# Kernel tuning notes

Measured on AMD Instinct MI355X. Metric: run time of the kernel, lower is better.

The kernel has to match this reference:

```python
import jax, jax.numpy as jnp
import numpy as np

B, N, D_IN, H, D_H, D_OUT = 2, 1024, 1024, 16, 64, 1024
NEG = -1e9


def skew_relative(QE_t):
    # QE_t: [B, H, N, 2N-1] -> [B, H, N, N] via the pad/reshape skew trick
    b, h, n = QE_t.shape[0], QE_t.shape[1], QE_t.shape[2]
    x = jnp.pad(QE_t, ((0, 0), (0, 0), (0, 0), (0, 1)))          # [B,H,N,2N]
    x = x.reshape(b, h, -1)                                       # [B,H,2N^2]
    x = jnp.pad(x, ((0, 0), (0, 0), (0, n - 1)))                  # [B,H,(N+1)(2N-1)]
    x = x.reshape(b, h, n + 1, 2 * n - 1)
    return x[:, :, :n, -n:]


def setup_inputs() -> dict:
    key = jax.random.key(0)
    ks = jax.random.split(key, 8)
    x = jax.random.normal(ks[0], (B, N, D_IN), dtype=jnp.float32)
    E_rel = jax.random.normal(ks[1], (2 * N - 1, D_H), dtype=jnp.float32)
    # additive causal mask [1,1,N,N]
    causal = jnp.tril(jnp.ones((N, N), dtype=bool))
    mask = jnp.where(causal, 0.0, NEG).astype(jnp.float32)[None, None]
    s = 1.0 / np.sqrt(D_IN)
    Wq = jax.random.normal(ks[2], (D_IN, H * D_H), dtype=jnp.float32) * s
    Wk = jax.random.normal(ks[3], (D_IN, H * D_H), dtype=jnp.float32) * s
    Wv = jax.random.normal(ks[4], (D_IN, H * D_H), dtype=jnp.float32) * s
    Wo = jax.random.normal(ks[5], (H * D_H, D_OUT), dtype=jnp.float32) * (1.0 / np.sqrt(H * D_H))
    bo = jnp.zeros((D_OUT,), dtype=jnp.float32)
    return {"x": x, "E_rel": E_rel, "mask": mask, "Wq": Wq, "Wk": Wk, "Wv": Wv, "Wo": Wo, "bo": bo}


def reference(x, E_rel, mask, Wq, Wk, Wv, Wo, bo):
    b = x.shape[0]
    scale = 1.0 / np.sqrt(D_H)
    # project and split heads -> [B, H, N, d]
    Q = (x @ Wq).reshape(b, -1, H, D_H).transpose(0, 2, 1, 3)
    K = (x @ Wk).reshape(b, -1, H, D_H).transpose(0, 2, 1, 3)
    V = (x @ Wv).reshape(b, -1, H, D_H).transpose(0, 2, 1, 3)
    attn = jnp.einsum('bhnd,bhmd->bhnm', Q, K)                    # [B,H,N,N]
    QE_t = jnp.einsum('bhnd,rd->bhnr', Q, E_rel)                  # [B,H,N,2N-1]
    attn = (attn + skew_relative(QE_t)) * scale + mask
    attn = jax.nn.softmax(attn, axis=-1)
    out = jnp.einsum('bhnm,bhmd->bhnd', attn, V)                  # [B,H,N,d]
    out = out.transpose(0, 2, 1, 3).reshape(b, -1, H * D_H)
    return out @ Wo + bo  # dropout is identity at inference
```

## Files before the change

kernel.cpp:

```cpp
#include <hip/hip_runtime.h>
#include <cstdint>
#include <cstddef>

typedef __bf16 bf16;
typedef __bf16 bf16x8 __attribute__((ext_vector_type(8)));
typedef float  f32x4  __attribute__((ext_vector_type(4)));

#define MFMA16(a,b,c) __builtin_amdgcn_mfma_f32_16x16x32_bf16((a),(b),(c),0,0,0)

__device__ __forceinline__ void gload_lds16(const bf16* g, bf16* l) {
  __builtin_amdgcn_global_load_lds((__attribute__((address_space(1))) void*)(g),
                                   (__attribute__((address_space(3))) void*)(l),
                                   16, 0, 0);
}

__global__ void cast_bf16_k(const float* __restrict__ src, bf16* __restrict__ dst, int n) {
  int i = (blockIdx.x * blockDim.x + threadIdx.x) * 4;
  if (i >= n) return;
  float4 v = *(const float4*)(src + i);
  dst[i + 0] = (bf16)v.x;
  dst[i + 1] = (bf16)v.y;
  dst[i + 2] = (bf16)v.z;
  dst[i + 3] = (bf16)v.w;
}

__global__ void transpose4_k(const float* __restrict__ W0, const float* __restrict__ W1,
                             const float* __restrict__ W2, const float* __restrict__ W3,
                             bf16* __restrict__ dst_base) {
  const int z = blockIdx.z;
  const float* src = (z == 0) ? W0 : (z == 1) ? W1 : (z == 2) ? W2 : W3;
  bf16* dst = dst_base + (size_t)z * (1024 * 1024);
  __shared__ float t[32][33];
  const int c0 = blockIdx.x * 32, r0 = blockIdx.y * 32;
  const int x = threadIdx.x, y = threadIdx.y;
  #pragma unroll
  for (int j = 0; j < 32; j += 8) t[y + j][x] = src[(size_t)(r0 + y + j) * 1024 + c0 + x];
  __syncthreads();
  #pragma unroll
  for (int j = 0; j < 32; j += 8)
    dst[(size_t)(c0 + y + j) * 1024 + r0 + x] = (bf16)t[x][y + j];
}

template <int NI>
__global__ __launch_bounds__(256) void gemm_k(
    const bf16* __restrict__ A, const bf16* __restrict__ Bt,
    bf16* __restrict__ QKV, float* __restrict__ Of,
    const float* __restrict__ bias, const int mode) {
  constexpr int K = 1024;
  const int row0 = blockIdx.x * 64;
  const int col0 = blockIdx.y * (NI * 64);

  __shared__ bf16 As[2][64 * 64];
  __shared__ bf16 Bs[2][NI * 64 * 64];

  const int tid = threadIdx.x;
  const int lane = tid & 63;
  const int wid = tid >> 6;
  const int lr = lane & 15;
  const int g  = lane >> 4;
  const int srow = lane >> 3;
  const int scol = ((lane & 7) ^ srow) * 8;

  f32x4 acc[4][NI];
  #pragma unroll
  for (int a = 0; a < 4; ++a)
    #pragma unroll
    for (int b = 0; b < NI; ++b) acc[a][b] = (f32x4){0.f, 0.f, 0.f, 0.f};

  auto stg = [&](int bb, int k0_) {
    #pragma unroll
    for (int q = 0; q < 2; ++q)
      gload_lds16(A + (size_t)(row0 + wid * 16 + q * 8 + srow) * K + k0_ + scol,
                  &As[bb][(wid * 16 + q * 8) * 64]);
    #pragma unroll
    for (int q = 0; q < 2 * NI; ++q)
      gload_lds16(Bt + (size_t)(col0 + wid * NI * 16 + q * 8 + srow) * K + k0_ + scol,
                  &Bs[bb][(wid * NI * 16 + q * 8) * 64]);
  };

  stg(0, 0);
  for (int t = 0; t < K / 64; ++t) {
    __syncthreads();
    if (t + 1 < K / 64) stg((t + 1) & 1, (t + 1) * 64);
    const bf16* as = &As[t & 1][0];
    const bf16* bs = &Bs[t & 1][0];
    bf16x8 af[4][2], bfv[NI][2];
    #pragma unroll
    for (int mi = 0; mi < 4; ++mi)
      #pragma unroll
      for (int kk = 0; kk < 2; ++kk)
        af[mi][kk] = *(const bf16x8*)&as[(mi * 16 + lr) * 64 + ((kk * 32 + g * 8) ^ ((lr & 7) << 3))];
    #pragma unroll
    for (int ni = 0; ni < NI; ++ni)
      #pragma unroll
      for (int kk = 0; kk < 2; ++kk)
        bfv[ni][kk] = *(const bf16x8*)&bs[(wid * NI * 16 + ni * 16 + lr) * 64 +
                                          ((kk * 32 + g * 8) ^ ((lr & 7) << 3))];
    #pragma unroll
    for (int mi = 0; mi < 4; ++mi)
      #pragma unroll
      for (int ni = 0; ni < NI; ++ni)
        #pragma unroll
        for (int kk = 0; kk < 2; ++kk)
          acc[mi][ni] = MFMA16(af[mi][kk], bfv[ni][kk], acc[mi][ni]);
  }

  #pragma unroll
  for (int mi = 0; mi < 4; ++mi) {
    #pragma unroll
    for (int ni = 0; ni < NI; ++ni) {
      #pragma unroll
      for (int r = 0; r < 4; ++r) {
        const int row = row0 + mi * 16 + g * 4 + r;
        const int col = col0 + wid * NI * 16 + ni * 16 + lr;
        const float v = acc[mi][ni][r];
        if (mode == 2) {
          Of[(size_t)row * 1024 + col] = v + bias[col];
        } else {
          const int b = row >> 10, i = row & 1023;
          const int which = col >> 10, cc = col & 1023;
          const int h = cc >> 6, d = cc & 63;
          if (which < 2)
            QKV[(size_t)which * 2097152 + (((size_t)(b * 16 + h)) * 1024 + i) * 64 + d] = (bf16)v;
          else
            QKV[(size_t)2 * 2097152 + (((size_t)(b * 16 + h)) * 64 + d) * 1024 + i] = (bf16)v;
        }
      }
    }
  }
}

__device__ const int CH_QB[36] = {7,7,7,7,7,7,7, 6,6,6,6,6,6, 5,5,5,5,5, 4,4,4,4,
                                  3,3,3, 2,2, 1, 0,1,2,3,4,5,6,7};
__device__ const int CH_K0[36] = {0,2,4,6,8,10,12, 0,2,4,6,8,10, 0,2,4,6,8, 0,2,4,6,
                                  0,2,4, 0,2, 0, 0,2,4,6,8,10,12,14};
__device__ const int QB_P0[8] = {0,1,3,6,10,15,21,28};

__global__ __launch_bounds__(512, 6) void attn_kernel(
    const bf16* __restrict__ Qh, const bf16* __restrict__ Kh,
    const bf16* __restrict__ Vt, const bf16* __restrict__ Eb,
    float* __restrict__ OP, float* __restrict__ LP) {
  constexpr int N = 1024;
  const int flat = blockIdx.y * 36 + blockIdx.x;
  const int task = (flat & 7) * 144 + (flat >> 3);
  const int bh = task / 36;
  const int ch = task - bh * 36;
  const int qb = CH_QB[ch];
  const int kb0 = CH_K0[ch];
  const int i0 = qb * 128;

  const bf16* Qp = Qh + (size_t)bh * N * 64;
  const bf16* Kp = Kh + (size_t)bh * N * 64;
  const bf16* Vp = Vt + (size_t)bh * 64 * N;

  __shared__ bf16 Ks[64 * 64];
  __shared__ bf16 Vs[64 * 64];
  __shared__ bf16 Es[192 * 64];

  const int tid = threadIdx.x;
  const int lane = tid & 63;
  const int wid = tid >> 6;
  const int lr = lane & 15;
  const int g  = lane >> 4;
  const int iw0 = i0 + wid * 16;
  bf16* pp = &Es[(wid * 16) * 64];

  const int srow8 = lane >> 3;
  const int sch = ((lane & 7) ^ srow8) * 8;

  bf16x8 qf[2];
  {
    const bf16* qrow = Qp + (size_t)(iw0 + lr) * 64 + g * 8;
    qf[0] = *(const bf16x8*)(qrow);
    qf[1] = *(const bf16x8*)(qrow + 32);
  }

  float lb[4] = {0.f, 0.f, 0.f, 0.f};
  f32x4 oacc[4];
  #pragma unroll
  for (int r = 0; r < 4; ++r) oacc[r] = (f32x4){0.f, 0.f, 0.f, 0.f};

  constexpr float SC = 0.18033688f;
  const int fb = 7 - wid;

  auto STAGE = [&](int j0) {
    gload_lds16(Kp + (size_t)(j0 + wid * 8 + srow8) * 64 + sch, &Ks[(wid * 8) * 64]);
    gload_lds16(Vp + (size_t)(wid * 8 + srow8) * 1024 + j0 + sch, &Vs[(wid * 8) * 64]);
    const int ebase = (N - 128) + j0 - i0;
    #pragma unroll
    for (int q = 0; q < 3; ++q)
      gload_lds16(Eb + (size_t)(ebase + wid * 24 + q * 8 + srow8) * 64 + sch,
                  &Es[(wid * 24 + q * 8) * 64]);
  };

  STAGE(kb0 * 64);
  __syncthreads();

  #pragma unroll
  for (int t = 0; t < 2; ++t) {
    const int j0 = (kb0 + t) * 64;
    const bool skip = (j0 > iw0 + 15);
    float p[4][4];
    if (!skip) {
      f32x4 sa[4];
      #pragma unroll
      for (int ni = 0; ni < 4; ++ni) sa[ni] = (f32x4){0.f, 0.f, 0.f, 0.f};
      __builtin_amdgcn_s_setprio(1);
      #pragma unroll
      for (int ni = 0; ni < 4; ++ni)
        #pragma unroll
        for (int kk = 0; kk < 2; ++kk) {
          bf16x8 kf = *(const bf16x8*)&Ks[(ni * 16 + lr) * 64 +
                                          ((kk * 32 + g * 8) ^ ((lr & 7) << 3))];
          sa[ni] = MFMA16(qf[kk], kf, sa[ni]);
        }
      f32x4 ea[5];
      #pragma unroll
      for (int s5 = 0; s5 < 5; ++s5) {
        const int er = (fb + s5) * 16 + lr;
        ea[s5] = (f32x4){0.f, 0.f, 0.f, 0.f};
        bf16x8 e0 = *(const bf16x8*)&Es[er * 64 + ((g * 8) ^ ((lr & 7) << 3))];
        bf16x8 e1 = *(const bf16x8*)&Es[er * 64 + ((32 + g * 8) ^ ((lr & 7) << 3))];
        ea[s5] = MFMA16(qf[0], e0, ea[s5]);
        ea[s5] = MFMA16(qf[1], e1, ea[s5]);
      }
      __builtin_amdgcn_s_setprio(0);
      #pragma unroll
      for (int r = 0; r < 4; ++r) {
        const int di = g * 4 + r;
        const int sl = (g << 4) | ((lr - di - 1) & 15);
        const float sh0 = __shfl(ea[0][r], sl);
        const float sh1 = __shfl(ea[1][r], sl);
        const float sh2 = __shfl(ea[2][r], sl);
        const float sh3 = __shfl(ea[3][r], sl);
        const float sh4 = __shfl(ea[4][r], sl);
        const bool hi = (lr > di);
        const float rel[4] = {hi ? sh1 : sh0, hi ? sh2 : sh1, hi ? sh3 : sh2, hi ? sh4 : sh3};
        const int ig = iw0 + di;
        #pragma unroll
        for (int ni = 0; ni < 4; ++ni) {
          float tv = (sa[ni][r] + rel[ni]) * SC;
          tv = (j0 + ni * 16 + lr > ig) ? -1e30f : tv;
          const float pv = exp2f(tv);
          lb[r] += pv;
          p[ni][r] = pv;
        }
      }
    }
    __syncthreads();
    if (!skip) {
      #pragma unroll
      for (int r = 0; r < 4; ++r) {
        const int di = g * 4 + r;
        #pragma unroll
        for (int ni = 0; ni < 4; ++ni)
          pp[di * 64 + ((ni * 16 + lr) ^ ((di & 7) << 3))] = (bf16)p[ni][r];
      }
      bf16x8 pf[2];
      pf[0] = *(const bf16x8*)&pp[lr * 64 + ((g * 8) ^ ((lr & 7) << 3))];
      pf[1] = *(const bf16x8*)&pp[lr * 64 + ((32 + g * 8) ^ ((lr & 7) << 3))];
      __builtin_amdgcn_s_setprio(1);
      #pragma unroll
      for (int nd = 0; nd < 4; ++nd)
        #pragma unroll
        for (int kk = 0; kk < 2; ++kk) {
          bf16x8 vf = *(const bf16x8*)&Vs[(nd * 16 + lr) * 64 +
                                          ((kk * 32 + g * 8) ^ ((lr & 7) << 3))];
          oacc[nd] = MFMA16(pf[kk], vf, oacc[nd]);
        }
      __builtin_amdgcn_s_setprio(0);
    }
    if (t == 0) {
      __syncthreads();
      STAGE(j0 + 64);
      __syncthreads();
    }
  }

  #pragma unroll
  for (int off = 1; off < 16; off <<= 1)
    #pragma unroll
    for (int r = 0; r < 4; ++r)
      lb[r] += __shfl_xor(lb[r], off);

  const int pslot = bh * 36 + QB_P0[qb] + (kb0 >> 1);
  float* Op = OP + (size_t)pslot * 8192;
  #pragma unroll
  for (int nd = 0; nd < 4; ++nd)
    #pragma unroll
    for (int r = 0; r < 4; ++r)
      Op[(size_t)(wid * 16 + g * 4 + r) * 64 + nd * 16 + lr] = oacc[nd][r];
  if (lr == 0) {
    #pragma unroll
    for (int r = 0; r < 4; ++r)
      LP[pslot * 128 + wid * 16 + g * 4 + r] = lb[r];
  }
}

__global__ __launch_bounds__(256) void merge_k(const float* __restrict__ OP,
                                               const float* __restrict__ LP,
                                               bf16* __restrict__ AO) {
  const int bh = blockIdx.x;
  const int qb = blockIdx.y;
  const int np = qb + 1;
  const int tid = threadIdx.x;
  const int row = tid >> 1;
  const int c0 = (tid & 1) * 32;
  const int p0 = bh * 36 + QB_P0[qb];

  float o[32];
  #pragma unroll
  for (int j = 0; j < 32; ++j) o[j] = 0.f;
  float l = 0.f;
  for (int c = 0; c < np; ++c) {
    l += LP[(p0 + c) * 128 + row];
    const float* Oc = OP + (size_t)(p0 + c) * 8192 + row * 64 + c0;
    #pragma unroll
    for (int j = 0; j < 32; j += 4) {
      const f32x4 v = *(const f32x4*)&Oc[j];
      o[j + 0] += v[0];
      o[j + 1] += v[1];
      o[j + 2] += v[2];
      o[j + 3] += v[3];
    }
  }
  const float inv = 1.f / l;

  const int b = bh >> 4, h = bh & 15;
  bf16* dst = AO + ((size_t)(b * 1024) + qb * 128 + row) * 1024 + h * 64 + c0;
  #pragma unroll
  for (int j = 0; j < 32; ++j) dst[j] = (bf16)(o[j] * inv);
}

extern "C" void kernel_launch(void* const* d_in, const int* in_sizes, int n_in,
                              void* d_out, int out_size, void* d_ws, size_t ws_size,
                              hipStream_t stream) {
  const float* x  = (const float*)d_in[0];
  const float* E  = (const float*)d_in[1];
  const float* Wq = (const float*)d_in[3];
  const float* Wk = (const float*)d_in[4];
  const float* Wv = (const float*)d_in[5];
  const float* Wo = (const float*)d_in[6];
  const float* bo = (const float*)d_in[7];

  bf16* xb  = (bf16*)d_ws;
  bf16* Wqt = xb + 2048 * 1024;
  bf16* Wot = Wqt + 3 * 1024 * 1024;
  bf16* Eb  = Wqt + 4 * 1024 * 1024;
  bf16* Qh  = Eb + 2048 * 64;
  bf16* AO  = Qh + 3 * 2048 * 1024;
  float* OP = (float*)(AO + 2048 * 1024);
  float* LPp = OP + (size_t)1152 * 8192;
  float* out = (float*)d_out;

  cast_bf16_k<<<dim3(2048), dim3(256), 0, stream>>>(x, xb, 2048 * 1024);
  cast_bf16_k<<<dim3(128), dim3(256), 0, stream>>>(E, Eb, 2047 * 64);
  transpose4_k<<<dim3(32, 32, 4), dim3(32, 8), 0, stream>>>(Wq, Wk, Wv, Wo, Wqt);

  gemm_k<2><<<dim3(32, 24), dim3(256), 0, stream>>>(xb, Wqt, Qh, nullptr, nullptr, 0);

  attn_kernel<<<dim3(36, 32), dim3(512), 0, stream>>>(
      Qh, Qh + 2048 * 1024, Qh + 2 * 2048 * 1024, Eb, OP, LPp);

  merge_k<<<dim3(32, 8), dim3(256), 0, stream>>>(OP, LPp, AO);

  gemm_k<2><<<dim3(32, 8), dim3(256), 0, stream>>>(AO, Wot, nullptr, out, bo, 2);
}
```

Before: 100.8 us.

## Fuse prep kernels, store attention partials in bf16, widen merge grid

Merges the x/E casts and the four weight transposes into one prep launch, which removes two kernel launches. Attention partial outputs are now written as bf16 instead of fp32, halving the partial-output traffic for the attention store and the merge load. The merge kernel gets twice as many blocks, each thread handling 16 columns, which adds parallelism. Rounding the unnormalized partial sums to bf16 before the merge adds precision loss.

```diff
diff --git a/kernel.cpp b/kernel.cpp
--- a/kernel.cpp
+++ b/kernel.cpp
@@ -14,31 +14,43 @@
                                    16, 0, 0);
 }
 
-__global__ void cast_bf16_k(const float* __restrict__ src, bf16* __restrict__ dst, int n) {
-  int i = (blockIdx.x * blockDim.x + threadIdx.x) * 4;
-  if (i >= n) return;
-  float4 v = *(const float4*)(src + i);
-  dst[i + 0] = (bf16)v.x;
-  dst[i + 1] = (bf16)v.y;
-  dst[i + 2] = (bf16)v.z;
-  dst[i + 3] = (bf16)v.w;
-}
-
-__global__ void transpose4_k(const float* __restrict__ W0, const float* __restrict__ W1,
-                             const float* __restrict__ W2, const float* __restrict__ W3,
-                             bf16* __restrict__ dst_base) {
-  const int z = blockIdx.z;
-  const float* src = (z == 0) ? W0 : (z == 1) ? W1 : (z == 2) ? W2 : W3;
-  bf16* dst = dst_base + (size_t)z * (1024 * 1024);
+__global__ __launch_bounds__(256) void prep_k(
+    const float* __restrict__ x, const float* __restrict__ E,
+    const float* __restrict__ W0, const float* __restrict__ W1,
+    const float* __restrict__ W2, const float* __restrict__ W3,
+    bf16* __restrict__ xb, bf16* __restrict__ Eb, bf16* __restrict__ Wt) {
   __shared__ float t[32][33];
-  const int c0 = blockIdx.x * 32, r0 = blockIdx.y * 32;
-  const int x = threadIdx.x, y = threadIdx.y;
-  #pragma unroll
-  for (int j = 0; j < 32; j += 8) t[y + j][x] = src[(size_t)(r0 + y + j) * 1024 + c0 + x];
-  __syncthreads();
-  #pragma unroll
-  for (int j = 0; j < 32; j += 8)
-    dst[(size_t)(c0 + y + j) * 1024 + r0 + x] = (bf16)t[x][y + j];
+  const int bid = blockIdx.x;
+  const int tid = threadIdx.x;
+  if (bid < 2176) {
+    const bool isx = (bid < 2048);
+    const float* src = isx ? x : E;
+    bf16* dst = isx ? xb : Eb;
+    const int n = isx ? (2048 * 1024) : (2047 * 64);
+    const int i = (isx ? bid : (bid - 2048)) * 1024 + tid * 4;
+    if (i < n) {
+      float4 v = *(const float4*)(src + i);
+      dst[i + 0] = (bf16)v.x;
+      dst[i + 1] = (bf16)v.y;
+      dst[i + 2] = (bf16)v.z;
+      dst[i + 3] = (bf16)v.w;
+    }
+  } else {
+    const int tt = bid - 2176;
+    const int z = tt >> 10;
+    const int rem = tt & 1023;
+    const int cx = (rem & 31) * 32;
+    const int ry = (rem >> 5) * 32;
+    const float* src = (z == 0) ? W0 : (z == 1) ? W1 : (z == 2) ? W2 : W3;
+    bf16* dst = Wt + (size_t)z * (1024 * 1024);
+    const int xx = tid & 31, yy = tid >> 5;
+    #pragma unroll
+    for (int j = 0; j < 32; j += 8) t[yy + j][xx] = src[(size_t)(ry + yy + j) * 1024 + cx + xx];
+    __syncthreads();
+    #pragma unroll
+    for (int j = 0; j < 32; j += 8)
+      dst[(size_t)(cx + yy + j) * 1024 + ry + xx] = (bf16)t[xx][yy + j];
+  }
 }
 
 template <int NI>
@@ -139,7 +151,7 @@
 __global__ __launch_bounds__(512, 6) void attn_kernel(
     const bf16* __restrict__ Qh, const bf16* __restrict__ Kh,
     const bf16* __restrict__ Vt, const bf16* __restrict__ Eb,
-    float* __restrict__ OP, float* __restrict__ LP) {
+    bf16* __restrict__ OP, float* __restrict__ LP) {
   constexpr int N = 1024;
   const int flat = blockIdx.y * 36 + blockIdx.x;
   const int task = (flat & 7) * 144 + (flat >> 3);
@@ -284,12 +296,12 @@
       lb[r] += __shfl_xor(lb[r], off);
 
   const int pslot = bh * 36 + QB_P0[qb] + (kb0 >> 1);
-  float* Op = OP + (size_t)pslot * 8192;
+  bf16* Op = OP + (size_t)pslot * 8192;
   #pragma unroll
   for (int nd = 0; nd < 4; ++nd)
     #pragma unroll
     for (int r = 0; r < 4; ++r)
-      Op[(size_t)(wid * 16 + g * 4 + r) * 64 + nd * 16 + lr] = oacc[nd][r];
+      Op[(size_t)(wid * 16 + g * 4 + r) * 64 + nd * 16 + lr] = (bf16)oacc[nd][r];
   if (lr == 0) {
     #pragma unroll
     for (int r = 0; r < 4; ++r)
@@ -297,31 +309,30 @@
   }
 }
 
-__global__ __launch_bounds__(256) void merge_k(const float* __restrict__ OP,
+__global__ __launch_bounds__(256) void merge_k(const bf16* __restrict__ OP,
                                                const float* __restrict__ LP,
                                                bf16* __restrict__ AO) {
   const int bh = blockIdx.x;
   const int qb = blockIdx.y;
+  const int half = blockIdx.z;
   const int np = qb + 1;
   const int tid = threadIdx.x;
-  const int row = tid >> 1;
-  const int c0 = (tid & 1) * 32;
+  const int row = half * 64 + (tid >> 2);
+  const int c0 = (tid & 3) * 16;
   const int p0 = bh * 36 + QB_P0[qb];
 
-  float o[32];
-  #pragma unroll
-  for (int j = 0; j < 32; ++j) o[j] = 0.f;
+  float o[16];
+  #pragma unroll
+  for (int j = 0; j < 16; ++j) o[j] = 0.f;
   float l = 0.f;
   for (int c = 0; c < np; ++c) {
     l += LP[(p0 + c) * 128 + row];
-    const float* Oc = OP + (size_t)(p0 + c) * 8192 + row * 64 + c0;
-    #pragma unroll
-    for (int j = 0; j < 32; j += 4) {
-      const f32x4 v = *(const f32x4*)&Oc[j];
-      o[j + 0] += v[0];
-      o[j + 1] += v[1];
-      o[j + 2] += v[2];
-      o[j + 3] += v[3];
+    const bf16* Oc = OP + (size_t)(p0 + c) * 8192 + row * 64 + c0;
+    #pragma unroll
+    for (int j = 0; j < 16; j += 8) {
+      const bf16x8 v = *(const bf16x8*)&Oc[j];
+      #pragma unroll
+      for (int u = 0; u < 8; ++u) o[j + u] += (float)v[u];
     }
   }
   const float inv = 1.f / l;
@@ -329,7 +340,7 @@
   const int b = bh >> 4, h = bh & 15;
   bf16* dst = AO + ((size_t)(b * 1024) + qb * 128 + row) * 1024 + h * 64 + c0;
   #pragma unroll
-  for (int j = 0; j < 32; ++j) dst[j] = (bf16)(o[j] * inv);
+  for (int j = 0; j < 16; ++j) dst[j] = (bf16)(o[j] * inv);
 }
 
 extern "C" void kernel_launch(void* const* d_in, const int* in_sizes, int n_in,
@@ -349,20 +360,18 @@
   bf16* Eb  = Wqt + 4 * 1024 * 1024;
   bf16* Qh  = Eb + 2048 * 64;
   bf16* AO  = Qh + 3 * 2048 * 1024;
-  float* OP = (float*)(AO + 2048 * 1024);
-  float* LPp = OP + (size_t)1152 * 8192;
+  bf16* OPb = AO + 2048 * 1024;
+  float* LPp = (float*)(OPb + (size_t)1152 * 8192);
   float* out = (float*)d_out;
 
-  cast_bf16_k<<<dim3(2048), dim3(256), 0, stream>>>(x, xb, 2048 * 1024);
-  cast_bf16_k<<<dim3(128), dim3(256), 0, stream>>>(E, Eb, 2047 * 64);
-  transpose4_k<<<dim3(32, 32, 4), dim3(32, 8), 0, stream>>>(Wq, Wk, Wv, Wo, Wqt);
+  prep_k<<<dim3(6272), dim3(256), 0, stream>>>(x, E, Wq, Wk, Wv, Wo, xb, Eb, Wqt);
 
   gemm_k<2><<<dim3(32, 24), dim3(256), 0, stream>>>(xb, Wqt, Qh, nullptr, nullptr, 0);
 
   attn_kernel<<<dim3(36, 32), dim3(512), 0, stream>>>(
-      Qh, Qh + 2048 * 1024, Qh + 2 * 2048 * 1024, Eb, OP, LPp);
-
-  merge_k<<<dim3(32, 8), dim3(256), 0, stream>>>(OP, LPp, AO);
+      Qh, Qh + 2048 * 1024, Qh + 2 * 2048 * 1024, Eb, OPb, LPp);
+
+  merge_k<<<dim3(32, 8, 2), dim3(256), 0, stream>>>(OPb, LPp, AO);
 
   gemm_k<2><<<dim3(32, 8), dim3(256), 0, stream>>>(AO, Wot, nullptr, out, bo, 2);
 }
```

Result: faster. 90.35 us (-10.4%).
